# Kernel optimization log

Measured on AMD Instinct MI355X. Metric: run time of the kernel, lower is better.

Reference implementation:

```python
import jax, jax.numpy as jnp
import numpy as np

B, L, D = 4, 2048, 1024
H = 4096          # hidden_units = 4*D
E = 8             # n_expert
K = 2             # n_expert_activated


def setup_inputs() -> dict:
    key = jax.random.key(0)
    k_x, k_g, k_w1, k_w2 = jax.random.split(key, 4)
    xs = jax.random.normal(k_x, (B, L, D), dtype=jnp.float32)
    gate_w = jax.random.normal(k_g, (E, D), dtype=jnp.float32) * 0.02   # Linear(D->E), no bias
    w1 = jax.random.normal(k_w1, (E, D, H), dtype=jnp.float32) * 0.02   # per-expert w_1 (bias=False)
    w2 = jax.random.normal(k_w2, (E, H, D), dtype=jnp.float32) * 0.02   # per-expert w_2 (bias=False)
    return {"xs": xs, "gate_w": gate_w, "w1": w1, "w2": w2}


def reference(xs, gate_w, w1, w2):
    b, l, d = xs.shape
    x = xs.reshape(-1, d)                                  # (N, D)
    n = x.shape[0]
    router = jnp.einsum('nd,ed->ne', x, gate_w)            # (N, E)
    logits, sel = jax.lax.top_k(router, K)                 # (N, K) each
    weights = jax.nn.softmax(logits.astype(jnp.float32), axis=-1).astype(x.dtype)
    # dense (N, E) combine weights: zero for unselected experts
    dense_w = jnp.zeros((n, E), dtype=x.dtype).at[jnp.arange(n)[:, None], sel].set(weights)
    # dense dispatch: run every expert on every token, zero-weight unselected.
    # Same math as the per-expert gather/scatter loop (dropout inactive at eval).
    h = jax.nn.relu(jnp.einsum('nd,edh->neh', x, w1))      # (N, E, H)
    out = jnp.einsum('neh,ehd,ne->nd', h, w2, dense_w)     # (N, D)
    return out.reshape(b, l, d)
```

## Files before the change

kernel.cpp:

```cpp
#include <hip/hip_runtime.h>
#include <hip/hip_bf16.h>

#define NTOK   8192
#define DDIM   1024
#define HDIM   4096
#define NEXP   8
#define CAP    8192
#define NSLOT  (NTOK * 2)

#define BM 128
#define BN 128
#define BK 64

typedef __attribute__((ext_vector_type(8))) short bf16x8;
typedef __attribute__((ext_vector_type(4))) float f32x4;

#define GLD16(g, l) __builtin_amdgcn_global_load_lds(                          \
    (const __attribute__((address_space(1))) void*)(g),                        \
    (__attribute__((address_space(3))) void*)(l), 16, 0, 0)

__global__ __launch_bounds__(64) void router_kernel(
    const float* __restrict__ xs, const float* __restrict__ gw,
    int* __restrict__ counts, int* __restrict__ toklist, float* __restrict__ wglist)
{
    const int n = blockIdx.x;
    const int lane = threadIdx.x;
    const float* xrow = xs + (size_t)n * DDIM;
    float xv[16];
#pragma unroll
    for (int j = 0; j < 16; ++j) xv[j] = xrow[lane + 64 * j];
    float logit[NEXP];
#pragma unroll
    for (int e = 0; e < NEXP; ++e) {
        float p = 0.f;
        const float* gr = gw + e * DDIM;
#pragma unroll
        for (int j = 0; j < 16; ++j) p += xv[j] * gr[lane + 64 * j];
#pragma unroll
        for (int off = 32; off >= 1; off >>= 1) p += __shfl_xor(p, off);
        logit[e] = p;
    }
    if (lane == 0) {
        int i0 = 0;
#pragma unroll
        for (int e = 1; e < NEXP; ++e) if (logit[e] > logit[i0]) i0 = e;
        int i1 = (i0 == 0) ? 1 : 0;
#pragma unroll
        for (int e = 0; e < NEXP; ++e) if (e != i0 && logit[e] > logit[i1]) i1 = e;
        float ex = expf(logit[i1] - logit[i0]);
        float w0 = 1.f / (1.f + ex);
        float w1 = ex * w0;
        int p0 = atomicAdd(&counts[i0], 1);
        toklist[i0 * CAP + p0] = n;
        wglist[i0 * CAP + p0] = w0;
        int p1 = atomicAdd(&counts[i1], 1);
        toklist[i1 * CAP + p1] = n;
        wglist[i1 * CAP + p1] = w1;
    }
}

__global__ void prefix_kernel(const int* __restrict__ counts, int* __restrict__ base)
{
    if (threadIdx.x == 0 && blockIdx.x == 0) {
        int s = 0;
        for (int e = 0; e < NEXP; ++e) { base[e] = s; s += counts[e]; }
    }
}

__global__ __launch_bounds__(256) void cvt_xs_kernel(
    const float* __restrict__ xs, __hip_bfloat16* __restrict__ xsb)
{
    const size_t i = ((size_t)blockIdx.x * 256 + threadIdx.x) * 8;
    const float4 a = *(const float4*)(xs + i);
    const float4 b = *(const float4*)(xs + i + 4);
    __hip_bfloat16 o[8];
    o[0] = __float2bfloat16(a.x); o[1] = __float2bfloat16(a.y);
    o[2] = __float2bfloat16(a.z); o[3] = __float2bfloat16(a.w);
    o[4] = __float2bfloat16(b.x); o[5] = __float2bfloat16(b.y);
    o[6] = __float2bfloat16(b.z); o[7] = __float2bfloat16(b.w);
    *(bf16x8*)(xsb + i) = *(bf16x8*)o;
}

__global__ __launch_bounds__(256) void transpose_bf16_kernel(
    const float* __restrict__ src, __hip_bfloat16* __restrict__ dst, int R, int C)
{
    __shared__ __hip_bfloat16 t[64][72];
    const int e = blockIdx.z;
    src += (size_t)e * R * C;
    dst += (size_t)e * R * C;
    const int r0 = blockIdx.y * 64, c0 = blockIdx.x * 64;
    const int tid = threadIdx.x;
#pragma unroll
    for (int i = 0; i < 4; ++i) {
        int r = (tid >> 4) + 16 * i;
        int c = (tid & 15) * 4;
        float4 v = *(const float4*)(src + (size_t)(r0 + r) * C + c0 + c);
        t[r][c + 0] = __float2bfloat16(v.x);
        t[r][c + 1] = __float2bfloat16(v.y);
        t[r][c + 2] = __float2bfloat16(v.z);
        t[r][c + 3] = __float2bfloat16(v.w);
    }
    __syncthreads();
#pragma unroll
    for (int i = 0; i < 4; ++i) {
        int c = (tid >> 4) + 16 * i;
        int r = (tid & 15) * 4;
        __hip_bfloat16 o[4] = { t[r][c], t[r + 1][c], t[r + 2][c], t[r + 3][c] };
        *(short4*)(dst + (size_t)(c0 + c) * R + r0 + r) = *(short4*)o;
    }
}

__global__ __launch_bounds__(256) void gemm1_kernel(
    const __hip_bfloat16* __restrict__ xsb, const __hip_bfloat16* __restrict__ w1t,
    const int* __restrict__ counts, const int* __restrict__ base,
    const int* __restrict__ toklist, __hip_bfloat16* __restrict__ h)
{
    const int e = blockIdx.z;
    const int cnt = counts[e];
    const int m0 = blockIdx.y * BM;
    if (m0 >= cnt) return;
    const int n0 = blockIdx.x * BN;

    __shared__ __align__(16) __hip_bfloat16 As[BM * BK];
    __shared__ __align__(16) __hip_bfloat16 Bs[BN * BK];
    __shared__ int tok_s[BM];

    const int tid = threadIdx.x;
    if (tid < BM) tok_s[tid] = toklist[e * CAP + min(m0 + tid, cnt - 1)];
    __syncthreads();

    const int wave = tid >> 6;
    const int lane = tid & 63;
    const int lrow = lane >> 3;
    const int lcol = (lane & 7) * 8;
    const __hip_bfloat16* w1e = w1t + (size_t)e * HDIM * DDIM;

    const __hip_bfloat16* srcA[4];
    const __hip_bfloat16* srcB[4];
#pragma unroll
    for (int c = 0; c < 4; ++c) {
        int r = wave * 32 + c * 8 + lrow;
        srcA[c] = xsb + (size_t)tok_s[r] * DDIM + lcol;
        srcB[c] = w1e + (size_t)(n0 + r) * DDIM + lcol;
    }

    f32x4 acc[4][4];
#pragma unroll
    for (int i = 0; i < 4; ++i)
#pragma unroll
        for (int j = 0; j < 4; ++j) acc[i][j] = (f32x4){0.f, 0.f, 0.f, 0.f};

    const int wm = (wave >> 1) * 64;
    const int wn = (wave & 1) * 64;
    const int l15 = lane & 15;
    const int quad = lane >> 4;

    for (int k0 = 0; k0 < DDIM; k0 += BK) {
#pragma unroll
        for (int c = 0; c < 4; ++c) {
            GLD16(srcA[c] + k0, As + (wave * 32 + c * 8) * BK);
            GLD16(srcB[c] + k0, Bs + (wave * 32 + c * 8) * BK);
        }
        __syncthreads();
#pragma unroll
        for (int kk = 0; kk < 2; ++kk) {
            bf16x8 a[4], b[4];
#pragma unroll
            for (int i = 0; i < 4; ++i)
                a[i] = *(const bf16x8*)(As + (wm + i * 16 + l15) * BK + kk * 32 + quad * 8);
#pragma unroll
            for (int j = 0; j < 4; ++j)
                b[j] = *(const bf16x8*)(Bs + (wn + j * 16 + l15) * BK + kk * 32 + quad * 8);
#pragma unroll
            for (int i = 0; i < 4; ++i)
#pragma unroll
                for (int j = 0; j < 4; ++j)
                    acc[i][j] = __builtin_amdgcn_mfma_f32_16x16x32_bf16(a[i], b[j], acc[i][j], 0, 0, 0);
        }
        __syncthreads();
    }

    const int slot0 = base[e] + m0;
#pragma unroll
    for (int i = 0; i < 4; ++i) {
#pragma unroll
        for (int r = 0; r < 4; ++r) {
            int row = wm + i * 16 + quad * 4 + r;
            if (m0 + row < cnt) {
                size_t hrow = (size_t)(slot0 + row) * HDIM + n0 + wn;
#pragma unroll
                for (int j = 0; j < 4; ++j)
                    h[hrow + j * 16 + l15] = __float2bfloat16(fmaxf(acc[i][j][r], 0.f));
            }
        }
    }
}

__global__ __launch_bounds__(256) void gemm2_kernel(
    const __hip_bfloat16* __restrict__ h, const __hip_bfloat16* __restrict__ w2t,
    const int* __restrict__ counts, const int* __restrict__ base,
    const int* __restrict__ toklist, const float* __restrict__ wglist,
    float* __restrict__ out)
{
    const int e = blockIdx.z;
    const int cnt = counts[e];
    const int m0 = blockIdx.y * BM;
    if (m0 >= cnt) return;
    const int n0 = blockIdx.x * BN;

    __shared__ __align__(16) __hip_bfloat16 As[BM * BK];
    __shared__ __align__(16) __hip_bfloat16 Bs[BN * BK];
    __shared__ int   tok_s[BM];
    __shared__ float wg_s[BM];

    const int tid = threadIdx.x;
    if (tid < BM) {
        int m = m0 + tid;
        tok_s[tid] = (m < cnt) ? toklist[e * CAP + m] : -1;
        wg_s[tid]  = (m < cnt) ? wglist[e * CAP + m] : 0.f;
    }
    __syncthreads();

    const int wave = tid >> 6;
    const int lane = tid & 63;
    const int lrow = lane >> 3;
    const int lcol = (lane & 7) * 8;
    const int slot0 = base[e];
    const __hip_bfloat16* w2e = w2t + (size_t)e * DDIM * HDIM;

    const __hip_bfloat16* srcA[4];
    const __hip_bfloat16* srcB[4];
#pragma unroll
    for (int c = 0; c < 4; ++c) {
        int r = wave * 32 + c * 8 + lrow;
        srcA[c] = h + (size_t)(slot0 + min(m0 + r, cnt - 1)) * HDIM + lcol;
        srcB[c] = w2e + (size_t)(n0 + r) * HDIM + lcol;
    }

    f32x4 acc[4][4];
#pragma unroll
    for (int i = 0; i < 4; ++i)
#pragma unroll
        for (int j = 0; j < 4; ++j) acc[i][j] = (f32x4){0.f, 0.f, 0.f, 0.f};

    const int wm = (wave >> 1) * 64;
    const int wn = (wave & 1) * 64;
    const int l15 = lane & 15;
    const int quad = lane >> 4;

    for (int k0 = 0; k0 < HDIM; k0 += BK) {
#pragma unroll
        for (int c = 0; c < 4; ++c) {
            GLD16(srcA[c] + k0, As + (wave * 32 + c * 8) * BK);
            GLD16(srcB[c] + k0, Bs + (wave * 32 + c * 8) * BK);
        }
        __syncthreads();
#pragma unroll
        for (int kk = 0; kk < 2; ++kk) {
            bf16x8 a[4], b[4];
#pragma unroll
            for (int i = 0; i < 4; ++i)
                a[i] = *(const bf16x8*)(As + (wm + i * 16 + l15) * BK + kk * 32 + quad * 8);
#pragma unroll
            for (int j = 0; j < 4; ++j)
                b[j] = *(const bf16x8*)(Bs + (wn + j * 16 + l15) * BK + kk * 32 + quad * 8);
#pragma unroll
            for (int i = 0; i < 4; ++i)
#pragma unroll
                for (int j = 0; j < 4; ++j)
                    acc[i][j] = __builtin_amdgcn_mfma_f32_16x16x32_bf16(a[i], b[j], acc[i][j], 0, 0, 0);
        }
        __syncthreads();
    }

#pragma unroll
    for (int i = 0; i < 4; ++i) {
#pragma unroll
        for (int r = 0; r < 4; ++r) {
            int row = wm + i * 16 + quad * 4 + r;
            if (m0 + row < cnt) {
                int tok = tok_s[row];
                float w = wg_s[row];
                float* orow = out + (size_t)tok * DDIM + n0 + wn;
#pragma unroll
                for (int j = 0; j < 4; ++j)
                    atomicAdd(&orow[j * 16 + l15], w * acc[i][j][r]);
            }
        }
    }
}

extern "C" void kernel_launch(void* const* d_in, const int* in_sizes, int n_in,
                              void* d_out, int out_size, void* d_ws, size_t ws_size,
                              hipStream_t stream)
{
    const float* xs = (const float*)d_in[0];
    const float* gw = (const float*)d_in[1];
    const float* w1 = (const float*)d_in[2];
    const float* w2 = (const float*)d_in[3];
    float* out = (float*)d_out;

    char* ws = (char*)d_ws;
    size_t o = 0;
    int*   counts  = (int*)(ws + o);  o += 256;
    int*   base    = (int*)(ws + o);  o += 256;
    int*   toklist = (int*)(ws + o);  o += (size_t)NEXP * CAP * 4;
    float* wglist  = (float*)(ws + o); o += (size_t)NEXP * CAP * 4;
    __hip_bfloat16* xsb = (__hip_bfloat16*)(ws + o); o += (size_t)NTOK * DDIM * 2;
    __hip_bfloat16* w1t = (__hip_bfloat16*)(ws + o); o += (size_t)NEXP * DDIM * HDIM * 2;
    __hip_bfloat16* w2t = (__hip_bfloat16*)(ws + o); o += (size_t)NEXP * DDIM * HDIM * 2;
    __hip_bfloat16* hbuf = (__hip_bfloat16*)(ws + o); o += (size_t)NSLOT * HDIM * 2;

    hipMemsetAsync(counts, 0, 256, stream);
    hipMemsetAsync(d_out, 0, (size_t)out_size * sizeof(float), stream);

    router_kernel<<<NTOK, 64, 0, stream>>>(xs, gw, counts, toklist, wglist);
    prefix_kernel<<<1, 64, 0, stream>>>(counts, base);
    cvt_xs_kernel<<<(NTOK * DDIM) / (256 * 8), 256, 0, stream>>>(xs, xsb);
    transpose_bf16_kernel<<<dim3(HDIM / 64, DDIM / 64, NEXP), 256, 0, stream>>>(w1, w1t, DDIM, HDIM);
    transpose_bf16_kernel<<<dim3(DDIM / 64, HDIM / 64, NEXP), 256, 0, stream>>>(w2, w2t, HDIM, DDIM);

    gemm1_kernel<<<dim3(HDIM / BN, CAP / BM, NEXP), 256, 0, stream>>>(
        xsb, w1t, counts, base, toklist, hbuf);
    gemm2_kernel<<<dim3(DDIM / BN, CAP / BM, NEXP), 256, 0, stream>>>(
        hbuf, w2t, counts, base, toklist, wglist, out);
}
```

Baseline: 1.100 ms.

## Replace grouped GEMMs with 256x256 double-buffered 8-wave pipelined MFMA kernel

The two grouped expert GEMMs become one templated kernel that uses 256x256 tiles and 8 waves. It double-buffers the LDS stages, interleaves global-to-LDS loads with MFMA phases under explicit waitcnt and barriers, and uses an XOR-swizzled LDS layout to avoid bank conflicts. It also remaps the 1D grid so consecutive blocks land on different experts, and raises MFMA priority with setprio. The aim is to hide load latency and raise MFMA utilisation, at the cost of heavy register pressure, larger tile padding waste for partially filled experts, and fragile hand-scheduled synchronisation.

```diff
diff --git a/kernel.cpp b/kernel.cpp
--- a/kernel.cpp
+++ b/kernel.cpp
@@ -7,10 +7,6 @@
 #define NEXP   8
 #define CAP    8192
 #define NSLOT  (NTOK * 2)
-
-#define BM 128
-#define BN 128
-#define BK 64
 
 typedef __attribute__((ext_vector_type(8))) short bf16x8;
 typedef __attribute__((ext_vector_type(4))) float f32x4;
@@ -110,183 +106,169 @@
     }
 }
 
-__global__ __launch_bounds__(256) void gemm1_kernel(
-    const __hip_bfloat16* __restrict__ xsb, const __hip_bfloat16* __restrict__ w1t,
-    const int* __restrict__ counts, const int* __restrict__ base,
-    const int* __restrict__ toklist, __hip_bfloat16* __restrict__ h)
-{
-    const int e = blockIdx.z;
-    const int cnt = counts[e];
-    const int m0 = blockIdx.y * BM;
-    if (m0 >= cnt) return;
-    const int n0 = blockIdx.x * BN;
-
-    __shared__ __align__(16) __hip_bfloat16 As[BM * BK];
-    __shared__ __align__(16) __hip_bfloat16 Bs[BN * BK];
-    __shared__ int tok_s[BM];
-
-    const int tid = threadIdx.x;
-    if (tid < BM) tok_s[tid] = toklist[e * CAP + min(m0 + tid, cnt - 1)];
-    __syncthreads();
-
-    const int wave = tid >> 6;
-    const int lane = tid & 63;
-    const int lrow = lane >> 3;
-    const int lcol = (lane & 7) * 8;
-    const __hip_bfloat16* w1e = w1t + (size_t)e * HDIM * DDIM;
-
-    const __hip_bfloat16* srcA[4];
-    const __hip_bfloat16* srcB[4];
-#pragma unroll
-    for (int c = 0; c < 4; ++c) {
-        int r = wave * 32 + c * 8 + lrow;
-        srcA[c] = xsb + (size_t)tok_s[r] * DDIM + lcol;
-        srcB[c] = w1e + (size_t)(n0 + r) * DDIM + lcol;
-    }
-
-    f32x4 acc[4][4];
-#pragma unroll
-    for (int i = 0; i < 4; ++i)
-#pragma unroll
-        for (int j = 0; j < 4; ++j) acc[i][j] = (f32x4){0.f, 0.f, 0.f, 0.f};
-
-    const int wm = (wave >> 1) * 64;
-    const int wn = (wave & 1) * 64;
-    const int l15 = lane & 15;
-    const int quad = lane >> 4;
-
-    for (int k0 = 0; k0 < DDIM; k0 += BK) {
-#pragma unroll
-        for (int c = 0; c < 4; ++c) {
-            GLD16(srcA[c] + k0, As + (wave * 32 + c * 8) * BK);
-            GLD16(srcB[c] + k0, Bs + (wave * 32 + c * 8) * BK);
-        }
-        __syncthreads();
-#pragma unroll
-        for (int kk = 0; kk < 2; ++kk) {
-            bf16x8 a[4], b[4];
-#pragma unroll
-            for (int i = 0; i < 4; ++i)
-                a[i] = *(const bf16x8*)(As + (wm + i * 16 + l15) * BK + kk * 32 + quad * 8);
-#pragma unroll
-            for (int j = 0; j < 4; ++j)
-                b[j] = *(const bf16x8*)(Bs + (wn + j * 16 + l15) * BK + kk * 32 + quad * 8);
-#pragma unroll
-            for (int i = 0; i < 4; ++i)
-#pragma unroll
-                for (int j = 0; j < 4; ++j)
-                    acc[i][j] = __builtin_amdgcn_mfma_f32_16x16x32_bf16(a[i], b[j], acc[i][j], 0, 0, 0);
-        }
-        __syncthreads();
-    }
-
-    const int slot0 = base[e] + m0;
-#pragma unroll
-    for (int i = 0; i < 4; ++i) {
-#pragma unroll
-        for (int r = 0; r < 4; ++r) {
-            int row = wm + i * 16 + quad * 4 + r;
-            if (m0 + row < cnt) {
-                size_t hrow = (size_t)(slot0 + row) * HDIM + n0 + wn;
-#pragma unroll
-                for (int j = 0; j < 4; ++j)
-                    h[hrow + j * 16 + l15] = __float2bfloat16(fmaxf(acc[i][j][r], 0.f));
-            }
-        }
-    }
-}
-
-__global__ __launch_bounds__(256) void gemm2_kernel(
-    const __hip_bfloat16* __restrict__ h, const __hip_bfloat16* __restrict__ w2t,
+
+#define BAR()   __builtin_amdgcn_s_barrier()
+#define LGKM0() do { asm volatile("s_waitcnt lgkmcnt(0)" ::: "memory"); \
+                     __builtin_amdgcn_sched_barrier(0); } while (0)
+#define VM2()   do { asm volatile("s_waitcnt vmcnt(2)" ::: "memory");   \
+                     __builtin_amdgcn_sched_barrier(0); } while (0)
+
+#define LDS_A(buf, mi, kk) \
+    (*(const bf16x8*)((const char*)(&As[buf][wr][0]) + (((mi) * 16 + l15) * 128) + cbk[kk]))
+#define LDS_B(buf, nj, kk) \
+    (*(const bf16x8*)((const char*)(&Bs[buf][bh][0]) + ((brow0 + (nj) * 16 + l15) * 128) + cbk[kk]))
+
+#define LDA4(buf, mib) do {                                              \
+    _Pragma("unroll") for (int i_ = 0; i_ < 4; ++i_) {                   \
+        aR[i_][0] = LDS_A(buf, (mib) + i_, 0);                           \
+        aR[i_][1] = LDS_A(buf, (mib) + i_, 1); } } while (0)
+
+#define LDB2(buf, njb) do {                                              \
+    _Pragma("unroll") for (int j_ = 0; j_ < 2; ++j_) {                   \
+        bR[(njb) + j_][0] = LDS_B(buf, (njb) + j_, 0);                   \
+        bR[(njb) + j_][1] = LDS_B(buf, (njb) + j_, 1); } } while (0)
+
+#define MFMA16(ib, jb) do {                                              \
+    __builtin_amdgcn_s_setprio(1);                                       \
+    _Pragma("unroll") for (int i_ = 0; i_ < 4; ++i_)                     \
+    _Pragma("unroll") for (int j_ = 0; j_ < 2; ++j_) {                   \
+        acc[(ib) + i_][(jb) + j_] = __builtin_amdgcn_mfma_f32_16x16x32_bf16( \
+            aR[i_][0], bR[(jb) + j_][0], acc[(ib) + i_][(jb) + j_], 0, 0, 0); \
+        acc[(ib) + i_][(jb) + j_] = __builtin_amdgcn_mfma_f32_16x16x32_bf16( \
+            aR[i_][1], bR[(jb) + j_][1], acc[(ib) + i_][(jb) + j_], 0, 0, 0); } \
+    __builtin_amdgcn_s_setprio(0); } while (0)
+
+#define STAGE(bb, hx, tt) do {                                           \
+    const int kb_ = min((tt), NT - 1) * 128;                             \
+    if ((hx) < 2) {                                                      \
+        GLD16(pA[hx][0] + kb_, &As[bb][hx][ldsr0]);                      \
+        GLD16(pA[hx][1] + kb_, &As[bb][hx][ldsr1]);                      \
+    } else {                                                             \
+        GLD16(pB[(hx) - 2][0] + kb_, &Bs[bb][(hx) - 2][ldsr0]);          \
+        GLD16(pB[(hx) - 2][1] + kb_, &Bs[bb][(hx) - 2][ldsr1]); } } while (0)
+
+template<int IS_G2>
+__global__ __launch_bounds__(512, 2) void gemm8p_kernel(
+    const __hip_bfloat16* __restrict__ Aglob, const __hip_bfloat16* __restrict__ Bglob,
     const int* __restrict__ counts, const int* __restrict__ base,
     const int* __restrict__ toklist, const float* __restrict__ wglist,
-    float* __restrict__ out)
-{
-    const int e = blockIdx.z;
+    __hip_bfloat16* __restrict__ hout, float* __restrict__ fout)
+{
+    constexpr int KD  = IS_G2 ? HDIM : DDIM;
+    constexpr int ND  = IS_G2 ? DDIM : HDIM;
+    constexpr int NT  = KD / 64;
+    constexpr int NTB = ND / 256;
+
+    const unsigned chunk = 32u * NTB;
+    const unsigned wg = (blockIdx.x & 7u) * chunk + (blockIdx.x >> 3);
+    const int e  = wg / chunk;
+    const unsigned rem = wg % chunk;
+    const int m0 = (int)(rem / NTB) * 256;
+    const int n0 = (int)(rem % NTB) * 256;
+
     const int cnt = counts[e];
-    const int m0 = blockIdx.y * BM;
     if (m0 >= cnt) return;
-    const int n0 = blockIdx.x * BN;
-
-    __shared__ __align__(16) __hip_bfloat16 As[BM * BK];
-    __shared__ __align__(16) __hip_bfloat16 Bs[BN * BK];
-    __shared__ int   tok_s[BM];
-    __shared__ float wg_s[BM];
-
-    const int tid = threadIdx.x;
-    if (tid < BM) {
-        int m = m0 + tid;
-        tok_s[tid] = (m < cnt) ? toklist[e * CAP + m] : -1;
-        wg_s[tid]  = (m < cnt) ? wglist[e * CAP + m] : 0.f;
-    }
-    __syncthreads();
-
-    const int wave = tid >> 6;
+
+    __shared__ __align__(16) __hip_bfloat16 As[2][2][128 * 64];
+    __shared__ __align__(16) __hip_bfloat16 Bs[2][2][128 * 64];
+
+    const int tid  = threadIdx.x;
+    const int wid  = tid >> 6;
     const int lane = tid & 63;
-    const int lrow = lane >> 3;
-    const int lcol = (lane & 7) * 8;
+    const int wr   = wid >> 2;
+    const int wc   = wid & 3;
+    const int bh   = wc >> 1;
+    const int brow0 = (wc & 1) * 64;
+    const int l15  = lane & 15;
+    const int quad = lane >> 4;
+
+    const int srow8 = lane >> 3;
+    const int cswz  = ((lane & 7) * 16) ^ (srow8 << 4);
+    const int ldsr0 = (wid * 16 + 0) * 64;
+    const int ldsr1 = (wid * 16 + 8) * 64;
+    const __hip_bfloat16* Be = Bglob + (size_t)e * ND * KD;
     const int slot0 = base[e];
-    const __hip_bfloat16* w2e = w2t + (size_t)e * DDIM * HDIM;
-
-    const __hip_bfloat16* srcA[4];
-    const __hip_bfloat16* srcB[4];
-#pragma unroll
-    for (int c = 0; c < 4; ++c) {
-        int r = wave * 32 + c * 8 + lrow;
-        srcA[c] = h + (size_t)(slot0 + min(m0 + r, cnt - 1)) * HDIM + lcol;
-        srcB[c] = w2e + (size_t)(n0 + r) * HDIM + lcol;
-    }
-
-    f32x4 acc[4][4];
-#pragma unroll
-    for (int i = 0; i < 4; ++i)
+
+    const char* pA[2][2];
+    const char* pB[2][2];
+#pragma unroll
+    for (int hh = 0; hh < 2; ++hh)
+#pragma unroll
+        for (int ii = 0; ii < 2; ++ii) {
+            const int lr = hh * 128 + wid * 16 + ii * 8 + srow8;
+            size_t arow;
+            if (IS_G2) arow = (size_t)(slot0 + min(m0 + lr, cnt - 1));
+            else       arow = (size_t)toklist[e * CAP + min(m0 + lr, cnt - 1)];
+            pA[hh][ii] = (const char*)(Aglob + arow * KD) + cswz;
+            pB[hh][ii] = (const char*)(Be + (size_t)(n0 + lr) * KD) + cswz;
+        }
+
+    int cbk[2];
+    cbk[0] = (quad * 16) ^ ((l15 & 7) << 4);
+    cbk[1] = (64 + quad * 16) ^ ((l15 & 7) << 4);
+
+    f32x4 acc[8][4];
+#pragma unroll
+    for (int i = 0; i < 8; ++i)
 #pragma unroll
         for (int j = 0; j < 4; ++j) acc[i][j] = (f32x4){0.f, 0.f, 0.f, 0.f};
-
-    const int wm = (wave >> 1) * 64;
-    const int wn = (wave & 1) * 64;
-    const int l15 = lane & 15;
-    const int quad = lane >> 4;
-
-    for (int k0 = 0; k0 < HDIM; k0 += BK) {
-#pragma unroll
-        for (int c = 0; c < 4; ++c) {
-            GLD16(srcA[c] + k0, As + (wave * 32 + c * 8) * BK);
-            GLD16(srcB[c] + k0, Bs + (wave * 32 + c * 8) * BK);
-        }
-        __syncthreads();
-#pragma unroll
-        for (int kk = 0; kk < 2; ++kk) {
-            bf16x8 a[4], b[4];
-#pragma unroll
-            for (int i = 0; i < 4; ++i)
-                a[i] = *(const bf16x8*)(As + (wm + i * 16 + l15) * BK + kk * 32 + quad * 8);
-#pragma unroll
-            for (int j = 0; j < 4; ++j)
-                b[j] = *(const bf16x8*)(Bs + (wn + j * 16 + l15) * BK + kk * 32 + quad * 8);
-#pragma unroll
-            for (int i = 0; i < 4; ++i)
-#pragma unroll
-                for (int j = 0; j < 4; ++j)
-                    acc[i][j] = __builtin_amdgcn_mfma_f32_16x16x32_bf16(a[i], b[j], acc[i][j], 0, 0, 0);
-        }
-        __syncthreads();
-    }
-
-#pragma unroll
-    for (int i = 0; i < 4; ++i) {
-#pragma unroll
-        for (int r = 0; r < 4; ++r) {
-            int row = wm + i * 16 + quad * 4 + r;
-            if (m0 + row < cnt) {
-                int tok = tok_s[row];
-                float w = wg_s[row];
-                float* orow = out + (size_t)tok * DDIM + n0 + wn;
-#pragma unroll
-                for (int j = 0; j < 4; ++j)
-                    atomicAdd(&orow[j * 16 + l15], w * acc[i][j][r]);
+    bf16x8 aR[4][2], bR[4][2];
+
+    STAGE(0, 0, 0); STAGE(0, 1, 0); STAGE(0, 2, 0); STAGE(0, 3, 0);
+    STAGE(1, 0, 1);
+    VM2();
+    BAR();
+
+#pragma unroll 1
+    for (int it = 0; it < NT / 2; ++it) {
+        const int T = 2 * it;
+        LDA4(0, 0); LDB2(0, 0); STAGE(1, 1, T + 1);
+        BAR(); LGKM0(); MFMA16(0, 0); BAR();
+        LDB2(0, 2); STAGE(1, 2, T + 1);
+        BAR(); LGKM0(); MFMA16(0, 2); BAR();
+        LDA4(0, 4); STAGE(1, 3, T + 1);
+        BAR(); LGKM0(); MFMA16(4, 2); BAR();
+        STAGE(0, 0, T + 2); VM2();
+        BAR(); MFMA16(4, 0); BAR();
+        LDA4(1, 0); LDB2(1, 0); STAGE(0, 1, T + 2);
+        BAR(); LGKM0(); MFMA16(0, 0); BAR();
+        LDB2(1, 2); STAGE(0, 2, T + 2);
+        BAR(); LGKM0(); MFMA16(0, 2); BAR();
+        LDA4(1, 4); STAGE(0, 3, T + 2);
+        BAR(); LGKM0(); MFMA16(4, 2); BAR();
+        STAGE(1, 0, T + 3); VM2();
+        BAR(); MFMA16(4, 0); BAR();
+    }
+
+    if (IS_G2) {
+#pragma unroll
+        for (int mi = 0; mi < 8; ++mi)
+#pragma unroll
+            for (int r = 0; r < 4; ++r) {
+                const int row = wr * 128 + mi * 16 + quad * 4 + r;
+                if (m0 + row < cnt) {
+                    const int tok   = toklist[e * CAP + m0 + row];
+                    const float wgt = wglist[e * CAP + m0 + row];
+                    float* orow = fout + (size_t)tok * DDIM + n0 + wc * 64;
+#pragma unroll
+                    for (int nj = 0; nj < 4; ++nj)
+                        atomicAdd(&orow[nj * 16 + l15], wgt * acc[mi][nj][r]);
+                }
             }
-        }
+    } else {
+#pragma unroll
+        for (int mi = 0; mi < 8; ++mi)
+#pragma unroll
+            for (int r = 0; r < 4; ++r) {
+                const int row = wr * 128 + mi * 16 + quad * 4 + r;
+                if (m0 + row < cnt) {
+                    size_t orow = (size_t)(slot0 + m0 + row) * HDIM + n0 + wc * 64;
+#pragma unroll
+                    for (int nj = 0; nj < 4; ++nj)
+                        hout[orow + nj * 16 + l15] =
+                            __float2bfloat16(fmaxf(acc[mi][nj][r], 0.f));
+                }
+            }
     }
 }
 
@@ -320,8 +302,8 @@
     transpose_bf16_kernel<<<dim3(HDIM / 64, DDIM / 64, NEXP), 256, 0, stream>>>(w1, w1t, DDIM, HDIM);
     transpose_bf16_kernel<<<dim3(DDIM / 64, HDIM / 64, NEXP), 256, 0, stream>>>(w2, w2t, HDIM, DDIM);
 
-    gemm1_kernel<<<dim3(HDIM / BN, CAP / BM, NEXP), 256, 0, stream>>>(
-        xsb, w1t, counts, base, toklist, hbuf);
-    gemm2_kernel<<<dim3(DDIM / BN, CAP / BM, NEXP), 256, 0, stream>>>(
-        hbuf, w2t, counts, base, toklist, wglist, out);
-}
+    gemm8p_kernel<0><<<NEXP * 32 * (HDIM / 256), 512, 0, stream>>>(
+        xsb, w1t, counts, base, toklist, wglist, hbuf, nullptr);
+    gemm8p_kernel<1><<<NEXP * 32 * (DDIM / 256), 512, 0, stream>>>(
+        hbuf, w2t, counts, base, toklist, wglist, nullptr, out);
+}
```

After: 1.040 ms. 1.06x faster.
